# Kernel optimization log

Measured on AMD Instinct MI355X. Metric: run time of the kernel, lower is better.

The kernel has to match this reference:

```python
import jax, jax.numpy as jnp
import numpy as np

KERNEL_SIZE = 11
SIGMA = 1.5
DATA_RANGE = 1.0
C1 = (0.01 * DATA_RANGE) ** 2
C2 = (0.03 * DATA_RANGE) ** 2


def _gaussian_kernel_2d(kernel_size=KERNEL_SIZE, sigma=SIGMA):
    coords = jnp.arange(kernel_size, dtype=jnp.float32) - kernel_size // 2
    g1d = jnp.exp(-coords ** 2 / (2.0 * sigma ** 2))
    g2d = g1d[:, None] * g1d[None, :]
    return g2d / g2d.sum()  # [K, K]


def _depthwise_blur(x, kernel2d):
    # x: [B, C, H, W]; kernel2d: [K, K] -> depthwise conv, SAME padding
    C = x.shape[1]
    k = jnp.broadcast_to(kernel2d[None, None], (C, 1, KERNEL_SIZE, KERNEL_SIZE)).astype(x.dtype)
    pad = KERNEL_SIZE // 2
    return jax.lax.conv_general_dilated(
        x, k,
        window_strides=(1, 1),
        padding=((pad, pad), (pad, pad)),
        dimension_numbers=('NCHW', 'OIHW', 'NCHW'),
        feature_group_count=C,
    )


def reference(pred, target):
    kernel2d = _gaussian_kernel_2d()
    mu_p = _depthwise_blur(pred, kernel2d)
    mu_t = _depthwise_blur(target, kernel2d)
    mu_p_sq = mu_p * mu_p
    mu_t_sq = mu_t * mu_t
    mu_pt = mu_p * mu_t
    sigma_p_sq = _depthwise_blur(pred * pred, kernel2d) - mu_p_sq
    sigma_t_sq = _depthwise_blur(target * target, kernel2d) - mu_t_sq
    sigma_pt = _depthwise_blur(pred * target, kernel2d) - mu_pt
    sigma_p_sq = jnp.clip(sigma_p_sq, 0.0, None)
    sigma_t_sq = jnp.clip(sigma_t_sq, 0.0, None)
    numerator = (2.0 * mu_pt + C1) * (2.0 * sigma_pt + C2)
    denominator = (mu_p_sq + mu_t_sq + C1) * (sigma_p_sq + sigma_t_sq + C2)
    ssim_map = numerator / denominator
    return 1.0 - jnp.mean(ssim_map)


def setup_inputs() -> dict:
    key = jax.random.key(0)
    k1, k2 = jax.random.split(key)
    shape = (16, 3, 512, 512)
    pred = jax.random.uniform(k1, shape, dtype=jnp.float32)
    target = jax.random.uniform(k2, shape, dtype=jnp.float32)
    return {"pred": pred, "target": target}
```

## Files before the change

### kernel.cpp

```cpp
#include <hip/hip_runtime.h>
#include <hip/hip_fp16.h>


#define WIDTH  512
#define HEIGHT 512
#define TW 64
#define SH 128
#define RING 48
#define ROWB 512
#define TILES_X 8
#define TILES_Y (HEIGHT / SH)
#define PLANES 48
#define NBLK (TILES_X * TILES_Y * PLANES)
#define NPIXF 12582912.0f

__device__ __forceinline__ void hblur_pack_store(const float* __restrict__ w,
                                                 const float* __restrict__ p,
                                                 const float* __restrict__ t,
                                                 __half* __restrict__ dst) {
    float aa[4] = {0,0,0,0}, ab[4] = {0,0,0,0},
          au[4] = {0,0,0,0}, av[4] = {0,0,0,0};
#pragma unroll
    for (int m = 3; m <= 16; ++m) {
        float pm = p[m], tm = t[m];
        float vm = pm * tm;
        float um = fmaf(pm, pm, tm * tm);
#pragma unroll
        for (int k = 0; k < 4; ++k) {
            int i = m - 3 - k;
            if (i >= 0 && i <= 10) {
                float wi = w[i];
                aa[k] = fmaf(wi, pm, aa[k]);
                ab[k] = fmaf(wi, tm, ab[k]);
                au[k] = fmaf(wi, um, au[k]);
                av[k] = fmaf(wi, vm, av[k]);
            }
        }
    }
    union { __half2 h2[8]; uint4 u4[2]; } pk;
#pragma unroll
    for (int k = 0; k < 4; ++k) {
        pk.h2[2*k+0] = __floats2half2_rn(aa[k], ab[k]);
        pk.h2[2*k+1] = __floats2half2_rn(au[k], av[k]);
    }
    ((uint4*)dst)[0] = pk.u4[0];
    ((uint4*)dst)[1] = pk.u4[1];
}

__device__ __forceinline__ void hblur_row_global(
    const float* __restrict__ P, const float* __restrict__ T,
    int x0, int gy, int cg, bool x_int, const float* __restrict__ w,
    __half* __restrict__ dst) {
    float p[20], t[20];
    if ((unsigned)gy >= (unsigned)HEIGHT) {
#pragma unroll
        for (int i = 0; i < 20; ++i) { p[i] = 0.f; t[i] = 0.f; }
    } else {
        const float* Pr = P + (size_t)gy * WIDTH;
        const float* Tr = T + (size_t)gy * WIDTH;
        const int gx0 = x0 + cg * 4 - 8;
        if (x_int) {
            const float4* Pq = (const float4*)(Pr + gx0);
            const float4* Tq = (const float4*)(Tr + gx0);
#pragma unroll
            for (int v = 0; v < 5; ++v) {
                float4 a = Pq[v], b = Tq[v];
                p[4*v+0] = a.x; p[4*v+1] = a.y; p[4*v+2] = a.z; p[4*v+3] = a.w;
                t[4*v+0] = b.x; t[4*v+1] = b.y; t[4*v+2] = b.z; t[4*v+3] = b.w;
            }
        } else {
#pragma unroll
            for (int i = 0; i < 20; ++i) {
                int gx = gx0 + i;
                bool ok = (unsigned)gx < (unsigned)WIDTH;
                p[i] = ok ? Pr[gx] : 0.f;
                t[i] = ok ? Tr[gx] : 0.f;
            }
        }
    }
    hblur_pack_store(w, p, t, dst);
}

__global__ __launch_bounds__(256)
void ssim_main(const float* __restrict__ pred,
               const float* __restrict__ tgt,
               float* __restrict__ partial) {
    __shared__ __half s_h[RING][TW][4];
    __shared__ float s_raw[2][2][16][80];
    __shared__ float s_red[4];

    const int tid = threadIdx.x;
    const int x0 = blockIdx.x * TW;
    const int y0 = blockIdx.y * SH;
    const size_t plane_off = (size_t)blockIdx.z * (WIDTH * HEIGHT);
    const float* P = pred + plane_off;
    const float* T = tgt + plane_off;
    const bool x_int = (x0 >= 8) && (x0 + TW + 8 <= WIDTH);

    const float w[11] = {0.00102839f, 0.00759881f, 0.03600077f, 0.10936069f,
                         0.21300566f, 0.26601168f, 0.21300566f, 0.10936069f,
                         0.03600077f, 0.00759881f, 0.00102839f};

    const int wv   = tid >> 6;
    const int lane = tid & 63;
    const int r1   = tid >> 4;
    const int cg1  = tid & 15;
    const int c    = tid & 63;
    const int rr   = (tid >> 6) << 2;

    auto issue_async = [&](int buf, int gybase) {
#pragma unroll 1
        for (int l = wv; l < 10; l += 4) {
            int fi  = l * 256 + lane * 4;
            int arr = fi / 1280;
            int rem = fi - arr * 1280;
            int row = rem / 80;
            int col = rem - row * 80;
            int gy = gybase + row; if (gy > HEIGHT - 1) gy = HEIGHT - 1;
            int gx = x0 - 8 + col;
            if (gx < 0) gx = 0;
            if (gx > WIDTH - 4) gx = WIDTH - 4;
            const float* src = (arr == 0 ? P : T) + ((size_t)gy << 9) + gx;
            char* ldsbase = (char*)&s_raw[buf][0][0][0] + l * 1024;
            __builtin_amdgcn_global_load_lds(
                (const __attribute__((address_space(1))) unsigned int*)(const void*)src,
                (__attribute__((address_space(3))) unsigned int*)(void*)ldsbase,
                16, 0, 0);
        }
    };

    issue_async(0, y0 + 21);
#pragma unroll 1
    for (int it = tid; it < 26 * 16; it += 256) {
        int r = it >> 4, cg = it & 15;
        hblur_row_global(P, T, x0, y0 - 5 + r, cg, x_int, w, &s_h[r][cg * 4][0]);
    }
    __syncthreads();

    float lsum = 0.f;

#pragma unroll 1
    for (int j = 0; j < SH / 16; ++j) {
        if (j < 6) issue_async((j + 1) & 1, y0 + 16 * j + 37);

        if (j < 7) {
            const int gy = y0 + 16 * j + 21 + r1;
            const int buf = j & 1;
            float p[20], t[20];
            const float4* rp = (const float4*)&s_raw[buf][0][r1][cg1 * 4];
            const float4* rt = (const float4*)&s_raw[buf][1][r1][cg1 * 4];
#pragma unroll
            for (int v = 0; v < 5; ++v) {
                float4 a = rp[v], b = rt[v];
                p[4*v+0] = a.x; p[4*v+1] = a.y; p[4*v+2] = a.z; p[4*v+3] = a.w;
                t[4*v+0] = b.x; t[4*v+1] = b.y; t[4*v+2] = b.z; t[4*v+3] = b.w;
            }
            if (!x_int || gy > HEIGHT - 1) {
                const int gx0 = x0 + cg1 * 4 - 8;
                const bool row_ok = gy <= HEIGHT - 1;
#pragma unroll
                for (int i = 0; i < 20; ++i) {
                    bool ok = row_ok && ((unsigned)(gx0 + i) < (unsigned)WIDTH);
                    if (!ok) { p[i] = 0.f; t[i] = 0.f; }
                }
            }
            int s = 16 * j + 26 + r1;
            if (s >= RING) s -= RING;
            if (s >= RING) s -= RING;
            hblur_pack_store(w, p, t, &s_h[s][cg1 * 4][0]);
        }

        {
            int s0 = 16 * j + rr;
            if (s0 >= RING) s0 -= RING;
            if (s0 >= RING) s0 -= RING;
            const int kwrap = RING - s0;
            const char* base = (const char*)&s_h[0][0][0];
            const int offA = s0 * ROWB + c * 8;
            const int offB = offA - RING * ROWB;

            float a4[4] = {0,0,0,0}, b4[4] = {0,0,0,0},
                  u4[4] = {0,0,0,0}, v4[4] = {0,0,0,0};
#pragma unroll
            for (int m = 0; m < 14; ++m) {
                const uint2 d = *(const uint2*)(base + (m < kwrap ? offA : offB)
                                                + m * ROWB);
                const float2 f0 = __half22float2(__builtin_bit_cast(__half2, d.x));
                const float2 f1 = __half22float2(__builtin_bit_cast(__half2, d.y));
#pragma unroll
                for (int r = 0; r < 4; ++r) {
                    int i = m - r;
                    if (i >= 0 && i <= 10) {
                        float wi = w[i];
                        a4[r] = fmaf(wi, f0.x, a4[r]);
                        b4[r] = fmaf(wi, f0.y, b4[r]);
                        u4[r] = fmaf(wi, f1.x, u4[r]);
                        v4[r] = fmaf(wi, f1.y, v4[r]);
                    }
                }
            }
#pragma unroll
            for (int r = 0; r < 4; ++r) {
                float mp = a4[r], mt = b4[r];
                float mpt = mp * mt;
                float B = fmaf(mp, mp, mt * mt);
                float spt  = v4[r] - mpt;
                float ssum = u4[r] - B;
                float num = (2.f * mpt + 1e-4f) * (2.f * spt + 9e-4f);
                float den = (B + 1e-4f) * (ssum + 9e-4f);
                lsum += __fdividef(num, den);
            }
        }

        __syncthreads();
    }

#pragma unroll
    for (int off = 32; off > 0; off >>= 1) lsum += __shfl_down(lsum, off);
    if ((tid & 63) == 0) s_red[tid >> 6] = lsum;
    __syncthreads();
    if (tid == 0) {
        partial[(blockIdx.z * TILES_Y + blockIdx.y) * TILES_X + blockIdx.x] =
            s_red[0] + s_red[1] + s_red[2] + s_red[3];
    }
}

__global__ __launch_bounds__(256)
void ssim_final(const float* __restrict__ partial, float* __restrict__ out) {
    __shared__ float s_red[4];
    float s = 0.f;
    for (int i = threadIdx.x; i < NBLK; i += 256) s += partial[i];
#pragma unroll
    for (int off = 32; off > 0; off >>= 1) s += __shfl_down(s, off);
    if ((threadIdx.x & 63) == 0) s_red[threadIdx.x >> 6] = s;
    __syncthreads();
    if (threadIdx.x == 0) {
        float total = s_red[0] + s_red[1] + s_red[2] + s_red[3];
        out[0] = 1.0f - total / NPIXF;
    }
}

extern "C" void kernel_launch(void* const* d_in, const int* in_sizes, int n_in,
                              void* d_out, int out_size, void* d_ws, size_t ws_size,
                              hipStream_t stream) {
    const float* pred = (const float*)d_in[0];
    const float* tgt  = (const float*)d_in[1];
    float* partial = (float*)d_ws;

    dim3 grid(TILES_X, TILES_Y, PLANES);
    ssim_main<<<grid, dim3(256), 0, stream>>>(pred, tgt, partial);
    ssim_final<<<1, dim3(256), 0, stream>>>(partial, (float*)d_out);
}
```

Baseline: 163.2 us.

## Shrink pipeline step to 8 rows with a 32-row power-of-two ring

Each iteration of the streaming pipeline now handles 8 output rows instead of 16. The shared ring buffer drops from 48 to 32 rows, so slot indices are computed with a mask, and the raw staging buffer is halved. Each thread computes 2 vertical outputs instead of 4, and only half the threads run the horizontal blur each step. This lowers LDS use, which may allow more resident blocks, and shortens the prologue. The cost is twice as many barriers and iterations, less register reuse in the vertical pass, and half the threads sitting idle during the horizontal stage.

```diff
diff --git a/kernel.cpp b/kernel.cpp
--- a/kernel.cpp
+++ b/kernel.cpp
@@ -6,7 +6,9 @@
 #define HEIGHT 512
 #define TW 64
 #define SH 128
-#define RING 48
+#define STEP 8
+#define NSTEP (SH / STEP)
+#define RING 32
 #define ROWB 512
 #define TILES_X 8
 #define TILES_Y (HEIGHT / SH)
@@ -86,7 +88,7 @@
                const float* __restrict__ tgt,
                float* __restrict__ partial) {
     __shared__ __half s_h[RING][TW][4];
-    __shared__ float s_raw[2][2][16][80];
+    __shared__ float s_raw[2][2][STEP][80];
     __shared__ float s_red[4];
 
     const int tid = threadIdx.x;
@@ -103,17 +105,17 @@
 
     const int wv   = tid >> 6;
     const int lane = tid & 63;
-    const int r1   = tid >> 4;
+    const int r1   = (tid >> 4) & 7;
     const int cg1  = tid & 15;
     const int c    = tid & 63;
-    const int rr   = (tid >> 6) << 2;
+    const int rr   = (tid >> 6) << 1;
 
     auto issue_async = [&](int buf, int gybase) {
 #pragma unroll 1
-        for (int l = wv; l < 10; l += 4) {
+        for (int l = wv; l < 5; l += 4) {
             int fi  = l * 256 + lane * 4;
-            int arr = fi / 1280;
-            int rem = fi - arr * 1280;
+            int arr = fi / 640;
+            int rem = fi - arr * 640;
             int row = rem / 80;
             int col = rem - row * 80;
             int gy = gybase + row; if (gy > HEIGHT - 1) gy = HEIGHT - 1;
@@ -129,9 +131,9 @@
         }
     };
 
-    issue_async(0, y0 + 21);
+    issue_async(0, y0 + STEP + 5);
 #pragma unroll 1
-    for (int it = tid; it < 26 * 16; it += 256) {
+    for (int it = tid; it < 18 * 16; it += 256) {
         int r = it >> 4, cg = it & 15;
         hblur_row_global(P, T, x0, y0 - 5 + r, cg, x_int, w, &s_h[r][cg * 4][0]);
     }
@@ -140,11 +142,11 @@
     float lsum = 0.f;
 
 #pragma unroll 1
-    for (int j = 0; j < SH / 16; ++j) {
-        if (j < 6) issue_async((j + 1) & 1, y0 + 16 * j + 37);
-
-        if (j < 7) {
-            const int gy = y0 + 16 * j + 21 + r1;
+    for (int j = 0; j < NSTEP; ++j) {
+        if (j < NSTEP - 2) issue_async((j + 1) & 1, y0 + STEP * (j + 1) + 13);
+
+        if (j < NSTEP - 1 && tid < 128) {
+            const int gy = y0 + STEP * j + 13 + r1;
             const int buf = j & 1;
             float p[20], t[20];
             const float4* rp = (const float4*)&s_raw[buf][0][r1][cg1 * 4];
@@ -164,48 +166,43 @@
                     if (!ok) { p[i] = 0.f; t[i] = 0.f; }
                 }
             }
-            int s = 16 * j + 26 + r1;
-            if (s >= RING) s -= RING;
-            if (s >= RING) s -= RING;
+            const int s = (STEP * j + 18 + r1) & (RING - 1);
             hblur_pack_store(w, p, t, &s_h[s][cg1 * 4][0]);
         }
 
         {
-            int s0 = 16 * j + rr;
-            if (s0 >= RING) s0 -= RING;
-            if (s0 >= RING) s0 -= RING;
+            const int s0 = (STEP * j + rr) & (RING - 1);
             const int kwrap = RING - s0;
             const char* base = (const char*)&s_h[0][0][0];
             const int offA = s0 * ROWB + c * 8;
             const int offB = offA - RING * ROWB;
 
-            float a4[4] = {0,0,0,0}, b4[4] = {0,0,0,0},
-                  u4[4] = {0,0,0,0}, v4[4] = {0,0,0,0};
-#pragma unroll
-            for (int m = 0; m < 14; ++m) {
+            float a2[2] = {0,0}, b2[2] = {0,0}, u2[2] = {0,0}, v2[2] = {0,0};
+#pragma unroll
+            for (int m = 0; m < 12; ++m) {
                 const uint2 d = *(const uint2*)(base + (m < kwrap ? offA : offB)
                                                 + m * ROWB);
                 const float2 f0 = __half22float2(__builtin_bit_cast(__half2, d.x));
                 const float2 f1 = __half22float2(__builtin_bit_cast(__half2, d.y));
 #pragma unroll
-                for (int r = 0; r < 4; ++r) {
+                for (int r = 0; r < 2; ++r) {
                     int i = m - r;
                     if (i >= 0 && i <= 10) {
                         float wi = w[i];
-                        a4[r] = fmaf(wi, f0.x, a4[r]);
-                        b4[r] = fmaf(wi, f0.y, b4[r]);
-                        u4[r] = fmaf(wi, f1.x, u4[r]);
-                        v4[r] = fmaf(wi, f1.y, v4[r]);
+                        a2[r] = fmaf(wi, f0.x, a2[r]);
+                        b2[r] = fmaf(wi, f0.y, b2[r]);
+                        u2[r] = fmaf(wi, f1.x, u2[r]);
+                        v2[r] = fmaf(wi, f1.y, v2[r]);
                     }
                 }
             }
 #pragma unroll
-            for (int r = 0; r < 4; ++r) {
-                float mp = a4[r], mt = b4[r];
+            for (int r = 0; r < 2; ++r) {
+                float mp = a2[r], mt = b2[r];
                 float mpt = mp * mt;
                 float B = fmaf(mp, mp, mt * mt);
-                float spt  = v4[r] - mpt;
-                float ssum = u4[r] - B;
+                float spt  = v2[r] - mpt;
+                float ssum = u2[r] - B;
                 float num = (2.f * mpt + 1e-4f) * (2.f * spt + 9e-4f);
                 float den = (B + 1e-4f) * (ssum + 9e-4f);
                 lsum += __fdividef(num, den);
```

Measured after the change: 170.6 us. 1.05x slower.
